# Optimization experiments

Measured on AMD Instinct MI355X. Metric: run time of the kernel, lower is better.

The kernel has to match this reference:

```python
import jax, jax.numpy as jnp
import numpy as np

SPLIT_LEVELS = 3
START_DIM = 0
GROUPS = 8
NUM_RECTS = 2 ** SPLIT_LEVELS


def setup_inputs() -> dict:
    key = jax.random.key(0)
    ks = jax.random.split(key, 10)
    B, N, C, Cin, H, W = 8, 2048, 512, 128, 96, 96
    sd = 0.02
    return {
        'x': jax.random.normal(ks[0], (B, N, C), jnp.float32),
        'r': jax.random.uniform(ks[1], (B, N, 4), jnp.float32),
        'I': jax.random.normal(ks[2], (B, Cin, H, W), jnp.float32),
        'IX': jax.random.normal(ks[3], (B, Cin, H, W), jnp.float32),
        'IY': jax.random.normal(ks[4], (B, Cin, H, W), jnp.float32),
        'IT': jax.random.normal(ks[5], (B, Cin, H, W), jnp.float32),
        'W_ratios': jax.random.normal(ks[6], (C, 2 ** SPLIT_LEVELS - 1), jnp.float32) * sd,
        'b_ratios': jnp.zeros((2 ** SPLIT_LEVELS - 1,), jnp.float32),
        'W_mask': jax.random.normal(ks[7], (C, NUM_RECTS * GROUPS), jnp.float32) * sd,
        'b_mask': jnp.zeros((NUM_RECTS * GROUPS,), jnp.float32),
        'W_samp': jax.random.normal(ks[8], (Cin, C), jnp.float32) * sd,
        'b_samp': jnp.zeros((C,), jnp.float32),
        'ln_g': jnp.ones((C,), jnp.float32),
        'ln_b': jnp.zeros((C,), jnp.float32),
    }


def _topleft(I, IX, IY, IT, x, y):
    # x, y: [B, P] continuous coords; returns [B, Cin, P]
    B, P = x.shape
    Cin = I.shape[1]
    x = x[:, None, :]
    y = y[:, None, :]
    X = jnp.ceil(x).astype(jnp.int32)
    Y = jnp.ceil(y).astype(jnp.int32)
    # torch uses X-1 (wraps at -1) but the matching weight is 0 there, so clamp is equivalent
    Xm = jnp.maximum(X - 1, 0)
    Ym = jnp.maximum(Y - 1, 0)
    z = jnp.zeros_like(X)
    dx = X.astype(x.dtype) - x
    dy = Y.astype(y.dtype) - y
    wx1 = 0.5 * dx ** 2
    wx2 = dx - wx1
    wy1 = 0.5 * dy ** 2
    wy2 = dy - wy1
    b = jnp.arange(B)[:, None, None]
    c = jnp.arange(Cin)[None, :, None]
    g = lambda A, xi, yi: A[b, c, xi, yi]  # gather -> [B, Cin, P]
    s_a = g(IT, X, Y)
    s_e1 = (wy1 * (g(IX, X, Ym) - 0.5 * g(I, X, Ym) - 0.5 * g(I, z, Ym))
            + wy2 * (g(IX, X, Y) - 0.5 * g(I, X, Y) - 0.5 * g(I, z, Y)))
    s_e2 = (wx1 * (g(IY, Xm, Y) - 0.5 * g(I, Xm, Y) - 0.5 * g(I, Xm, z))
            + wx2 * (g(IY, X, Y) - 0.5 * g(I, X, Y) - 0.5 * g(I, X, z)))
    s_c = (wx1 * wy1 * g(I, Xm, Ym) + wx2 * wy1 * g(I, X, Ym)
           + wx1 * wy2 * g(I, Xm, Y) + wx2 * wy2 * g(I, X, Y))
    return s_a - s_e1 - s_e2 + s_c


def _sample_rects(r, I, IX, IY, IT):
    # r: [B, M, rects, 4] normalized rects
    B, M, rects, _ = r.shape
    Cin, H, W = I.shape[1], I.shape[2], I.shape[3]
    fac = jnp.array([H - 1, W - 1, H - 1, W - 1], dtype=r.dtype)
    p = (r * fac).reshape(B, M * rects, 4)
    x1, y1, x2, y2 = p[..., 0], p[..., 1], p[..., 2], p[..., 3]
    tl = lambda xx, yy: _topleft(I, IX, IY, IT, xx, yy)
    S = tl(x2, y2) - tl(x1, y2) - tl(x2, y1) + tl(x1, y1)
    area = jnp.abs((x1 - x2) * (y1 - y2)) + 1e-9
    S = S / area[:, None, :]
    return S.reshape(B, Cin, M, rects).transpose(0, 2, 3, 1)  # [B, M, rects, Cin]


def _forward(x, r, I, IX, IY, IT, W_ratios, b_ratios, W_mask, b_mask, W_samp, b_samp, ln_g, ln_b):
    B, N, C = x.shape
    ratios = jax.nn.sigmoid(x @ W_ratios + b_ratios)  # [B, N, 2^L - 1]
    rr = r[:, :, None, :]  # [B, N, 1, 4]
    level_rects = []
    for i in range(SPLIT_LEVELS):
        dim = (START_DIM + i) % 2
        rat = ratios[:, :, 2 ** i - 1: 2 ** (i + 1) - 1][..., None]  # [B,N,2^i,1]
        p0, p1, p2, p3 = jnp.split(rr, 4, axis=3)
        pos = (p0, p1, p2, p3)
        mid = pos[dim] * (1 - rat) + pos[dim + 2] * rat
        if dim == 0:
            r1 = jnp.concatenate([p0, p1, mid, p3], 3)
            r2 = jnp.concatenate([mid, p1, p2, p3], 3)
        else:
            r1 = jnp.concatenate([p0, p1, p2, mid], 3)
            r2 = jnp.concatenate([p0, mid, p2, p3], 3)
        rr = jnp.concatenate([r1, r2], 2)
        level_rects.append(rr)
    mask = jax.nn.softmax((x @ W_mask + b_mask).reshape(B, N, NUM_RECTS, GROUPS), axis=2)
    S = _sample_rects(rr, I, IX, IY, IT)          # [B, N, rects, Cin]
    s = S @ W_samp + b_samp                        # [B, N, rects, C]
    gc = C // GROUPS
    s = s.reshape(B, N, NUM_RECTS, GROUPS, gc)
    y = jnp.einsum('bnsg,bnsgc->bngc', mask, s).reshape(B, N, C)
    mu = jnp.mean(y, axis=-1, keepdims=True)
    var = jnp.var(y, axis=-1, keepdims=True)
    y = (y - mu) / jnp.sqrt(var + 1e-5) * ln_g + ln_b + x
    return y, level_rects


def reference(x, r, I, IX, IY, IT, W_ratios, b_ratios, W_mask, b_mask, W_samp, b_samp, ln_g, ln_b):
    y, level_rects = _forward(x, r, I, IX, IY, IT, W_ratios, b_ratios, W_mask, b_mask,
                              W_samp, b_samp, ln_g, ln_b)
    return (y, *level_rects)
```

## Files before the change

kernel.cpp:

```cpp
#include <hip/hip_runtime.h>
#include <math.h>

#define B_    8
#define N_    2048
#define C_    512
#define CIN_  128
#define H_    96
#define W_    96
#define HW_   (H_*W_)
#define IMG_  (CIN_*HW_)

#define OUT_L0 (B_*N_*C_)
#define OUT_L1 (OUT_L0 + B_*N_*8)
#define OUT_L2 (OUT_L1 + B_*N_*16)

__device__ __forceinline__ float fm(float a, float b) { return __fmul_rn(a, b); }
__device__ __forceinline__ float fa(float a, float b) { return __fadd_rn(a, b); }
__device__ __forceinline__ float fs(float a, float b) { return __fsub_rn(a, b); }

#define TCH 64
__global__ __launch_bounds__(256) void transpose_kernel(
    const float* __restrict__ I, const float* __restrict__ IX,
    const float* __restrict__ IY, const float* __restrict__ IT,
    float* __restrict__ out)
{
    __shared__ float tile[TCH][97];
    const int x   = blockIdx.x;
    const int b   = blockIdx.y;
    const int z   = blockIdx.z;
    const int img = z >> 1;
    const int ch0 = (z & 1) * TCH;
    const float* src = (img == 0) ? I : (img == 1) ? IX : (img == 2) ? IY : IT;
    const float* sp = src + (size_t)b * IMG_ + (size_t)ch0 * HW_ + (size_t)x * W_;

    for (int i = threadIdx.x; i < TCH * 24; i += 256) {
        const int c = i / 24, qy = i - c * 24;
        const float4 v = *(const float4*)(sp + (size_t)c * HW_ + qy * 4);
        tile[c][qy * 4 + 0] = v.x; tile[c][qy * 4 + 1] = v.y;
        tile[c][qy * 4 + 2] = v.z; tile[c][qy * 4 + 3] = v.w;
    }
    __syncthreads();
    float* op = out + (size_t)img * (B_ * (size_t)HW_ * CIN_)
                    + (size_t)b * ((size_t)HW_ * CIN_)
                    + (size_t)x * (W_ * CIN_) + ch0;
    for (int i = threadIdx.x; i < 96 * 16; i += 256) {
        const int y = i >> 4, cq = i & 15;
        float4 w;
        w.x = tile[cq * 4 + 0][y]; w.y = tile[cq * 4 + 1][y];
        w.z = tile[cq * 4 + 2][y]; w.w = tile[cq * 4 + 3][y];
        *(float4*)(op + (size_t)y * CIN_ + cq * 4) = w;
    }
}

__global__ __launch_bounds__(256) void frontend_kernel(
    const float* __restrict__ x, const float* __restrict__ r,
    const float* __restrict__ Wr, const float* __restrict__ br,
    const float* __restrict__ Wm, const float* __restrict__ bm,
    float* __restrict__ out, float* __restrict__ rects_ws, float* __restrict__ mask_ws)
{
    const int wv   = threadIdx.x >> 6;
    const int lane = threadIdx.x & 63;
    const int row0 = blockIdx.x << 4;
    const int rb   = wv << 2;

    __shared__ __align__(16) float xs[16][C_];
    __shared__ float mlog[16][64];
    __shared__ float ratv[16][7];

    {
        const float4* xp = (const float4*)(x + (size_t)row0 * C_);
        float4* xd = (float4*)xs;
        #pragma unroll
        for (int i = 0; i < 8; ++i) xd[threadIdx.x + i * 256] = xp[threadIdx.x + i * 256];
    }
    __syncthreads();

    {
        const int o = lane;
        float p[4][4];
        #pragma unroll
        for (int rr = 0; rr < 4; ++rr)
            #pragma unroll
            for (int q = 0; q < 4; ++q) p[rr][q] = 0.f;
        #pragma unroll
        for (int q = 0; q < 4; ++q) {
            const float* wp = Wm + (size_t)(q * 128) * 64 + o;
            #pragma unroll 8
            for (int i = 0; i < 128; ++i) {
                const float wm = wp[(size_t)i * 64];
                p[0][q] = fmaf(xs[rb + 0][q * 128 + i], wm, p[0][q]);
                p[1][q] = fmaf(xs[rb + 1][q * 128 + i], wm, p[1][q]);
                p[2][q] = fmaf(xs[rb + 2][q * 128 + i], wm, p[2][q]);
                p[3][q] = fmaf(xs[rb + 3][q * 128 + i], wm, p[3][q]);
            }
        }
        #pragma unroll
        for (int rr = 0; rr < 4; ++rr)
            mlog[rb + rr][o] = fa(fa(fa(fa(p[rr][0], p[rr][1]), p[rr][2]), p[rr][3]), bm[o]);
    }
    if (lane < 32) {
        const int rr = lane >> 3, o = lane & 7;
        if (o < 7) {
            const float* wp = Wr + o;
            const float* xr = xs[rb + rr];
            float p1 = 0.f, p2 = 0.f;
            for (int k = 0; k < 384; ++k)   p1 = fmaf(xr[k], wp[(size_t)k * 7], p1);
            for (int k = 384; k < 512; ++k) p2 = fmaf(xr[k], wp[(size_t)k * 7], p2);
            const float z = fa(fa(p1, p2), br[o]);
            ratv[rb + rr][o] = (float)(1.0 / (1.0 + exp(-(double)z)));
        }
    }
    __syncthreads();

    if (threadIdx.x < 128) {
        const int rr = threadIdx.x >> 3, g = threadIdx.x & 7;
        float mx = -1e30f;
        #pragma unroll
        for (int s = 0; s < 8; ++s) mx = fmaxf(mx, mlog[rr][s * 8 + g]);
        float e[8], sum = 0.f;
        #pragma unroll
        for (int s = 0; s < 8; ++s) { e[s] = expf(mlog[rr][s * 8 + g] - mx); sum += e[s]; }
        const float inv = 1.0f / sum;
        float* mw = mask_ws + (size_t)(row0 + rr) * 64;
        #pragma unroll
        for (int s = 0; s < 8; ++s) mw[s * 8 + g] = e[s] * inv;
    } else if (threadIdx.x < 144) {
        const int rr  = threadIdx.x - 128;
        const int row = row0 + rr;
        float rx1[8], ry1[8], rx2[8], ry2[8];
        const float* rp = r + (size_t)row * 4;
        rx1[0] = rp[0]; ry1[0] = rp[1]; rx2[0] = rp[2]; ry2[0] = rp[3];
        float* lr0 = out + OUT_L0 + (size_t)row * 8;
        float* lr1 = out + OUT_L1 + (size_t)row * 16;
        float* lr2 = out + OUT_L2 + (size_t)row * 32;
        {
            const float t = ratv[rr][0];
            const float m = fa(fm(rx1[0], fs(1.0f, t)), fm(rx2[0], t));
            rx1[1] = m; ry1[1] = ry1[0]; rx2[1] = rx2[0]; ry2[1] = ry2[0];
            rx2[0] = m;
        }
        for (int s = 0; s < 2; ++s) {
            lr0[s*4+0] = rx1[s]; lr0[s*4+1] = ry1[s];
            lr0[s*4+2] = rx2[s]; lr0[s*4+3] = ry2[s];
        }
        for (int j = 0; j < 2; ++j) {
            const float t = ratv[rr][1 + j];
            const float m = fa(fm(ry1[j], fs(1.0f, t)), fm(ry2[j], t));
            rx1[2+j] = rx1[j]; ry1[2+j] = m; rx2[2+j] = rx2[j]; ry2[2+j] = ry2[j];
            ry2[j] = m;
        }
        for (int s = 0; s < 4; ++s) {
            lr1[s*4+0] = rx1[s]; lr1[s*4+1] = ry1[s];
            lr1[s*4+2] = rx2[s]; lr1[s*4+3] = ry2[s];
        }
        for (int j = 0; j < 4; ++j) {
            const float t = ratv[rr][3 + j];
            const float m = fa(fm(rx1[j], fs(1.0f, t)), fm(rx2[j], t));
            rx1[4+j] = m; ry1[4+j] = ry1[j]; rx2[4+j] = rx2[j]; ry2[4+j] = ry2[j];
            rx2[j] = m;
        }
        float* rw = rects_ws + (size_t)row * 32;
        for (int s = 0; s < 8; ++s) {
            lr2[s*4+0] = rx1[s]; lr2[s*4+1] = ry1[s];
            lr2[s*4+2] = rx2[s]; lr2[s*4+3] = ry2[s];
            rw[s*4+0] = rx1[s]; rw[s*4+1] = ry1[s];
            rw[s*4+2] = rx2[s]; rw[s*4+3] = ry2[s];
        }
    }
}

template <bool NHWC>
__device__ __forceinline__ float4 ld4f(const float* __restrict__ p, int xi, int yi, int c0)
{
    if (NHWC) {
        return *(const float4*)(p + ((size_t)(xi * W_ + yi) * CIN_ + c0));
    } else {
        const float* q = p + (size_t)c0 * HW_ + xi * W_ + yi;
        float4 v;
        v.x = q[0]; v.y = q[HW_]; v.z = q[2 * HW_]; v.w = q[3 * HW_];
        return v;
    }
}

__device__ __forceinline__ void sample_one(
    const float* __restrict__ rect, int c0,
    const float* __restrict__ pI, const float* __restrict__ pIX,
    const float* __restrict__ pIY, const float* __restrict__ pIT,
    float* __restrict__ Sout)
{
    const float X1 = fm(rect[0], 95.0f), Y1 = fm(rect[1], 95.0f);
    const float X2 = fm(rect[2], 95.0f), Y2 = fm(rect[3], 95.0f);
    const float area = fa(fabsf(fm(fs(X1, X2), fs(Y1, Y2))), 1e-9f);

    const float uxv[2] = { X2, X1 };
    const float uyv[2] = { Y2, Y1 };
    int UX[2], UXm[2], UY[2], UYm[2];
    float wx1u[2], wx2u[2], wy1u[2], wy2u[2];
    #pragma unroll
    for (int j = 0; j < 2; ++j) {
        const float xcf = ceilf(uxv[j]);
        UX[j] = (int)xcf; UXm[j] = max(UX[j] - 1, 0);
        const float dx = fs(xcf, uxv[j]);
        wx1u[j] = fm(0.5f, fm(dx, dx)); wx2u[j] = fs(dx, wx1u[j]);
        const float ycf = ceilf(uyv[j]);
        UY[j] = (int)ycf; UYm[j] = max(UY[j] - 1, 0);
        const float dy = fs(ycf, uyv[j]);
        wy1u[j] = fm(0.5f, fm(dy, dy)); wy2u[j] = fs(dy, wy1u[j]);
    }

    float4 i_xm0u[2], i_x0u[2], i_0ymu[2], i_0yu[2];
    #pragma unroll
    for (int j = 0; j < 2; ++j) {
        i_xm0u[j] = ld4f<true>(pI, UXm[j], 0, c0);
        i_x0u[j]  = ld4f<true>(pI, UX[j],  0, c0);
        i_0ymu[j] = ld4f<true>(pI, 0, UYm[j], c0);
        i_0yu[j]  = ld4f<true>(pI, 0, UY[j],  c0);
    }
    float4 it_xy[4], ix_xym[4], ix_xy[4], iy_xmy[4], iy_xy[4],
           i_xym[4], i_xy[4], i_xmy[4], i_xmym[4];
    #pragma unroll
    for (int k = 0; k < 4; ++k) {
        const int X = UX[k & 1], Xm = UXm[k & 1];
        const int Y = UY[k >> 1], Ym = UYm[k >> 1];
        it_xy[k]  = ld4f<true>(pIT, X,  Y,  c0);
        ix_xym[k] = ld4f<true>(pIX, X,  Ym, c0);
        ix_xy[k]  = ld4f<true>(pIX, X,  Y,  c0);
        iy_xmy[k] = ld4f<true>(pIY, Xm, Y,  c0);
        iy_xy[k]  = ld4f<true>(pIY, X,  Y,  c0);
        i_xym[k]  = ld4f<true>(pI,  X,  Ym, c0);
        i_xy[k]   = ld4f<true>(pI,  X,  Y,  c0);
        i_xmy[k]  = ld4f<true>(pI,  Xm, Y,  c0);
        i_xmym[k] = ld4f<true>(pI,  Xm, Ym, c0);
    }

    float4 tlv[4];
    #define TLF_BODY(k, f) { \
        const float wx1 = wx1u[(k) & 1], wx2 = wx2u[(k) & 1]; \
        const float wy1 = wy1u[(k) >> 1], wy2 = wy2u[(k) >> 1]; \
        const float t1 = fs(fs(ix_xym[k].f, fm(0.5f, i_xym[k].f)), fm(0.5f, i_0ymu[(k) >> 1].f)); \
        const float t2 = fs(fs(ix_xy[k].f,  fm(0.5f, i_xy[k].f)),  fm(0.5f, i_0yu[(k) >> 1].f)); \
        const float e1 = fa(fm(wy1, t1), fm(wy2, t2)); \
        const float u1 = fs(fs(iy_xmy[k].f, fm(0.5f, i_xmy[k].f)), fm(0.5f, i_xm0u[(k) & 1].f)); \
        const float u2 = fs(fs(iy_xy[k].f,  fm(0.5f, i_xy[k].f)),  fm(0.5f, i_x0u[(k) & 1].f)); \
        const float e2 = fa(fm(wx1, u1), fm(wx2, u2)); \
        const float cc = fa(fa(fa(fm(fm(wx1, wy1), i_xmym[k].f), \
                                   fm(fm(wx2, wy1), i_xym[k].f)), \
                                   fm(fm(wx1, wy2), i_xmy[k].f)), \
                                   fm(fm(wx2, wy2), i_xy[k].f)); \
        tlv[k].f = fa(fs(fs(it_xy[k].f, e1), e2), cc); }
    TLF_BODY(0, x) TLF_BODY(0, y) TLF_BODY(0, z) TLF_BODY(0, w)
    TLF_BODY(1, x) TLF_BODY(1, y) TLF_BODY(1, z) TLF_BODY(1, w)
    TLF_BODY(2, x) TLF_BODY(2, y) TLF_BODY(2, z) TLF_BODY(2, w)
    TLF_BODY(3, x) TLF_BODY(3, y) TLF_BODY(3, z) TLF_BODY(3, w)
    #undef TLF_BODY

    #define SCOMB(f, idx) { \
        const float sc = fa(fs(fs(tlv[0].f, tlv[1].f), tlv[2].f), tlv[3].f); \
        Sout[c0 + idx] = sc / area; }
    SCOMB(x, 0) SCOMB(y, 1) SCOMB(z, 2) SCOMB(w, 3)
    #undef SCOMB
}

__global__ __launch_bounds__(256) void gather5_kernel(
    const float* __restrict__ gI, const float* __restrict__ gIX,
    const float* __restrict__ gIY, const float* __restrict__ gIT,
    const float* __restrict__ rects_ws, const float* __restrict__ mask_ws,
    float* __restrict__ sm_ws)
{
    const int bid   = blockIdx.x;
    const int batch = bid & 7;
    const int row0  = (batch << 11) | ((bid >> 3) << 2);
    const int tid   = threadIdx.x;
    const int rr    = tid >> 6;
    const int c0    = (tid & 63) << 1;

    __shared__ float rect_l[4][32];
    __shared__ float mask_l[4][64];
    if (tid < 128) ((float*)rect_l)[tid] = rects_ws[(size_t)row0 * 32 + tid];
    ((float*)mask_l)[tid] = mask_ws[(size_t)row0 * 64 + tid];
    __syncthreads();

    const float* rl = rect_l[rr];
    const float xt[7] = { rl[0], rl[2], rl[18], rl[6], rl[22], rl[10], rl[14] };
    const float yt[4] = { rl[1], rl[3], rl[7], rl[11] };

    float Xf[7]; int Xc[7], Xm[7]; float wx1v[7], wx2v[7];
    #pragma unroll
    for (int i = 0; i < 7; ++i) {
        Xf[i] = fm(xt[i], 95.0f);
        const float cf = ceilf(Xf[i]);
        Xc[i] = (int)cf; Xm[i] = max(Xc[i] - 1, 0);
        const float dx = fs(cf, Xf[i]);
        wx1v[i] = fm(0.5f, fm(dx, dx)); wx2v[i] = fs(dx, wx1v[i]);
    }
    float Yf[4]; int Yc[4], Ymv[4]; float wy1v[4], wy2v[4];
    #pragma unroll
    for (int i = 0; i < 4; ++i) {
        Yf[i] = fm(yt[i], 95.0f);
        const float cf = ceilf(Yf[i]);
        Yc[i] = (int)cf; Ymv[i] = max(Yc[i] - 1, 0);
        const float dy = fs(cf, Yf[i]);
        wy1v[i] = fm(0.5f, fm(dy, dy)); wy2v[i] = fs(dy, wy1v[i]);
    }

    const size_t bb = (size_t)batch * IMG_;
    const float* pI  = gI  + bb;
    const float* pIX = gIX + bb;
    const float* pIY = gIY + bb;
    const float* pIT = gIT + bb;

    float2 tl[18];
    #define LD2(p, xi, yi) (*(const float2*)((p) + ((size_t)((xi) * W_ + (yi)) * CIN_ + c0)))
    #define TLC(P, f) { \
        const float t1 = fs(fs(ix_xym.f, fm(0.5f, i_xym.f)), fm(0.5f, i_0ym.f)); \
        const float t2 = fs(fs(ix_xy.f,  fm(0.5f, i_xy.f)),  fm(0.5f, i_0y.f)); \
        const float e1 = fa(fm(wy1, t1), fm(wy2, t2)); \
        const float u1 = fs(fs(iy_xmy.f, fm(0.5f, i_xmy.f)), fm(0.5f, i_xm0.f)); \
        const float u2 = fs(fs(iy_xy.f,  fm(0.5f, i_xy.f)),  fm(0.5f, i_x0.f)); \
        const float e2 = fa(fm(wx1, u1), fm(wx2, u2)); \
        const float cc = fa(fa(fa(fm(fm(wx1, wy1), i_xmym.f), \
                                   fm(fm(wx2, wy1), i_xym.f)), \
                                   fm(fm(wx1, wy2), i_xmy.f)), \
                                   fm(fm(wx2, wy2), i_xy.f)); \
        tl[P].f = fa(fs(fs(it_xy.f, e1), e2), cc); }
    #define PT(P, XI, YI) { \
        const int X = Xc[XI], Xmm = Xm[XI], Y = Yc[YI], Ymm = Ymv[YI]; \
        const float wx1 = wx1v[XI], wx2 = wx2v[XI], wy1 = wy1v[YI], wy2 = wy2v[YI]; \
        const float2 it_xy  = LD2(pIT, X,   Y); \
        const float2 ix_xym = LD2(pIX, X,   Ymm); \
        const float2 ix_xy  = LD2(pIX, X,   Y); \
        const float2 iy_xmy = LD2(pIY, Xmm, Y); \
        const float2 iy_xy  = LD2(pIY, X,   Y); \
        const float2 i_xym  = LD2(pI,  X,   Ymm); \
        const float2 i_0ym  = LD2(pI,  0,   Ymm); \
        const float2 i_xy   = LD2(pI,  X,   Y); \
        const float2 i_0y   = LD2(pI,  0,   Y); \
        const float2 i_xmy  = LD2(pI,  Xmm, Y); \
        const float2 i_xm0  = LD2(pI,  Xmm, 0); \
        const float2 i_x0   = LD2(pI,  X,   0); \
        const float2 i_xmym = LD2(pI,  Xmm, Ymm); \
        TLC(P, x) TLC(P, y) }

    PT(0, 0, 0) PT(1, 1, 0) PT(2, 2, 0) PT(5, 0, 1) PT(6, 1, 1) PT(7, 2, 1)
    PT(3, 3, 0) PT(4, 4, 0) PT(9, 2, 2) PT(10, 3, 2) PT(11, 4, 2)
    PT(8, 5, 1) PT(13, 0, 3) PT(14, 2, 3) PT(15, 5, 3)
    PT(12, 6, 2) PT(16, 6, 3) PT(17, 4, 3)
    #undef PT
    #undef TLC
    #undef LD2

    float2 S[8];
    #define AREA(x1i, y1i, x2i, y2i) \
        fa(fabsf(fm(fs(Xf[x1i], Xf[x2i]), fs(Yf[y1i], Yf[y2i]))), 1e-9f)
    #define COMB(s, A, Bp, Cp, D, x1i, y1i, x2i, y2i) { \
        const float ar = AREA(x1i, y1i, x2i, y2i); \
        S[s].x = fa(fs(fs(tl[A].x, tl[Bp].x), tl[Cp].x), tl[D].x) / ar; \
        S[s].y = fa(fs(fs(tl[A].y, tl[Bp].y), tl[Cp].y), tl[D].y) / ar; }
    COMB(0,  6,  5,  1,  0,  0, 0, 1, 1)
    COMB(1, 10,  9,  3,  2,  2, 0, 3, 2)
    COMB(2, 15, 13,  8,  5,  0, 1, 5, 3)
    COMB(3, 16, 14, 12,  9,  2, 2, 6, 3)
    COMB(4,  7,  6,  2,  1,  1, 0, 2, 1)
    COMB(5, 11, 10,  4,  3,  3, 0, 4, 2)
    COMB(6, 14, 15,  7,  8,  5, 1, 2, 3)
    COMB(7, 17, 16, 11, 12,  6, 2, 4, 3)
    #undef COMB
    #undef AREA

    const float* mk = mask_l[rr];
    float* smp = sm_ws + (size_t)(row0 + rr) * 1024 + c0;
    #pragma unroll
    for (int g = 0; g < 8; ++g) {
        float ax = 0.f, ay = 0.f;
        #pragma unroll
        for (int s = 0; s < 8; ++s) {
            const float m = mk[s * 8 + g];
            ax = fmaf(m, S[s].x, ax);
            ay = fmaf(m, S[s].y, ay);
        }
        *(float2*)(smp + g * 128) = make_float2(ax, ay);
    }
}

#define R78 16
__global__ __launch_bounds__(256) void stage78_kernel(
    const float* __restrict__ x,
    const float* __restrict__ Ws, const float* __restrict__ bs,
    const float* __restrict__ lng, const float* __restrict__ lnb,
    const float* __restrict__ sm_ws, float* __restrict__ out)
{
    const int row0 = blockIdx.x * R78;
    const int tid  = threadIdx.x;

    __shared__ __align__(16) float SM_l[R78][8][CIN_];
    __shared__ float red[R78][4][2];
    __shared__ float stats[R78][2];

    {
        const float4* src = (const float4*)(sm_ws + (size_t)row0 * 1024);
        float4* dst = (float4*)SM_l;
        #pragma unroll
        for (int k = 0; k < 16; ++k) dst[tid + k * 256] = src[tid + k * 256];
    }
    __syncthreads();

    const int o0 = tid, o1 = tid + 256;
    const int g0 = o0 >> 6, g1 = o1 >> 6;
    float a0[R78], a1[R78];
    {
        const float b0 = bs[o0], b1 = bs[o1];
        #pragma unroll
        for (int q = 0; q < R78; ++q) { a0[q] = b0; a1[q] = b1; }
    }
    const float* w0 = Ws + o0;
    #pragma unroll 4
    for (int c = 0; c < 128; ++c) {
        const float wa = w0[(size_t)c * 512];
        const float wb = w0[(size_t)c * 512 + 256];
        #pragma unroll
        for (int q = 0; q < R78; ++q) {
            a0[q] = fmaf(SM_l[q][g0][c], wa, a0[q]);
            a1[q] = fmaf(SM_l[q][g1][c], wb, a1[q]);
        }
    }
    const int wv = tid >> 6, lane = tid & 63;
    #pragma unroll
    for (int q = 0; q < R78; ++q) {
        float s1 = a0[q] + a1[q];
        float s2 = fmaf(a0[q], a0[q], a1[q] * a1[q]);
        #pragma unroll
        for (int off = 32; off > 0; off >>= 1) {
            s1 += __shfl_down(s1, off);
            s2 += __shfl_down(s2, off);
        }
        if (lane == 0) { red[q][wv][0] = s1; red[q][wv][1] = s2; }
    }
    __syncthreads();
    if (tid < R78) {
        float t1 = 0.f, t2 = 0.f;
        #pragma unroll
        for (int w = 0; w < 4; ++w) { t1 += red[tid][w][0]; t2 += red[tid][w][1]; }
        const float mu  = t1 * (1.0f / 512.0f);
        const float var = t2 * (1.0f / 512.0f) - mu * mu;
        stats[tid][0] = mu; stats[tid][1] = rsqrtf(var + 1e-5f);
    }
    __syncthreads();
    const float lg0 = lng[o0], lb0 = lnb[o0];
    const float lg1 = lng[o1], lb1 = lnb[o1];
    #pragma unroll
    for (int q = 0; q < R78; ++q) {
        const size_t rowb = (size_t)(row0 + q) * C_;
        const float mu = stats[q][0], rstd = stats[q][1];
        out[rowb + o0] = (a0[q] - mu) * rstd * lg0 + lb0 + x[rowb + o0];
        out[rowb + o1] = (a1[q] - mu) * rstd * lg1 + lb1 + x[rowb + o1];
    }
}

__global__ __launch_bounds__(512) void gather_kernel(
    const float* __restrict__ x,
    const float* __restrict__ Ws, const float* __restrict__ bs,
    const float* __restrict__ lng, const float* __restrict__ lnb,
    const float* __restrict__ gI, const float* __restrict__ gIX,
    const float* __restrict__ gIY, const float* __restrict__ gIT,
    const float* __restrict__ rects_ws, const float* __restrict__ mask_ws,
    float* __restrict__ out)
{
    const int bid   = blockIdx.x;
    const int batch = bid & 7;
    const int row0  = (batch << 11) | ((bid >> 3) << 2);
    const int tid   = threadIdx.x;

    __shared__ __align__(16) float xs[4][C_];
    __shared__ float mask_s[4][64];
    __shared__ float rects[4][8][4];
    __shared__ __align__(16) float S_s[4][8][CIN_];
    __shared__ __align__(16) float SM_s[4][8][CIN_];
    __shared__ __align__(16) float yv[4][C_];
    __shared__ float red2[4][8][2];
    __shared__ float stats[4][2];

    {
        const int rr = tid >> 7, q = tid & 127;
        ((float4*)xs[rr])[q] = ((const float4*)(x + (size_t)(row0 + rr) * C_))[q];
    }
    if (tid < 128)      ((float*)rects)[tid] = rects_ws[(size_t)row0 * 32 + tid];
    else if (tid < 384) ((float*)mask_s)[tid - 128] = mask_ws[(size_t)row0 * 64 + (tid - 128)];
    __syncthreads();

    {
        const size_t bb = (size_t)batch * IMG_;
        const float* pI  = gI  + bb;
        const float* pIX = gIX + bb;
        const float* pIY = gIY + bb;
        const float* pIT = gIT + bb;
        #pragma unroll
        for (int it = 0; it < 2; ++it) {
            const int t  = tid + (it << 9);
            const int rr = t >> 8;
            const int s  = (t >> 5) & 7;
            const int c0 = (t & 31) << 2;
            sample_one(rects[rr][s], c0, pI, pIX, pIY, pIT, S_s[rr][s]);
        }
    }
    __syncthreads();

    {
        const int rr = tid >> 7, c = tid & 127;
        #pragma unroll
        for (int g = 0; g < 8; ++g) {
            float acc = 0.f;
            #pragma unroll
            for (int s = 0; s < 8; ++s)
                acc = fmaf(mask_s[rr][s * 8 + g], S_s[rr][s][c], acc);
            SM_s[rr][g][c] = acc;
        }
    }
    __syncthreads();

    {
        const int o = tid;
        const int g = o >> 6;
        float a0 = bs[o], a1 = a0, a2 = a0, a3 = a0;
        const float* w0 = Ws + o;
        #pragma unroll 4
        for (int c = 0; c < 128; ++c) {
            const float w = w0[(size_t)c * 512];
            a0 = fmaf(SM_s[0][g][c], w, a0);
            a1 = fmaf(SM_s[1][g][c], w, a1);
            a2 = fmaf(SM_s[2][g][c], w, a2);
            a3 = fmaf(SM_s[3][g][c], w, a3);
        }
        yv[0][o] = a0; yv[1][o] = a1; yv[2][o] = a2; yv[3][o] = a3;
    }
    __syncthreads();

    {
        const int o = tid, wvv = tid >> 6, lane = tid & 63;
        float v[4], s1[4], s2[4];
        #pragma unroll
        for (int rr = 0; rr < 4; ++rr) {
            v[rr]  = yv[rr][o];
            s1[rr] = v[rr];
            s2[rr] = v[rr] * v[rr];
        }
        #pragma unroll
        for (int off = 32; off > 0; off >>= 1) {
            #pragma unroll
            for (int rr = 0; rr < 4; ++rr) {
                s1[rr] += __shfl_down(s1[rr], off);
                s2[rr] += __shfl_down(s2[rr], off);
            }
        }
        if (lane == 0) {
            #pragma unroll
            for (int rr = 0; rr < 4; ++rr) {
                red2[rr][wvv][0] = s1[rr];
                red2[rr][wvv][1] = s2[rr];
            }
        }
        __syncthreads();
        if (tid < 4) {
            float t1 = 0.f, t2 = 0.f;
            #pragma unroll
            for (int w = 0; w < 8; ++w) { t1 += red2[tid][w][0]; t2 += red2[tid][w][1]; }
            const float mu  = t1 * (1.0f / 512.0f);
            const float var = t2 * (1.0f / 512.0f) - mu * mu;
            stats[tid][0] = mu; stats[tid][1] = rsqrtf(var + 1e-5f);
        }
        __syncthreads();
        const float lg = lng[o], lb = lnb[o];
        #pragma unroll
        for (int rr = 0; rr < 4; ++rr) {
            out[(size_t)(row0 + rr) * C_ + o] =
                (v[rr] - stats[rr][0]) * stats[rr][1] * lg + lb + xs[rr][o];
        }
    }
}

template <bool NHWC>
__global__ __launch_bounds__(256) void fused_kernel(
    const float* __restrict__ x, const float* __restrict__ r,
    const float* __restrict__ Wr, const float* __restrict__ br,
    const float* __restrict__ Wm, const float* __restrict__ bm,
    const float* __restrict__ Ws, const float* __restrict__ bs,
    const float* __restrict__ lng, const float* __restrict__ lnb,
    const float* __restrict__ gI, const float* __restrict__ gIX,
    const float* __restrict__ gIY, const float* __restrict__ gIT,
    float* __restrict__ out)
{
    const int row = blockIdx.x;
    const int b   = row >> 11;
    const int tid = threadIdx.x;

    __shared__ __align__(16) float xs[C_];
    __shared__ float mpart[4][64];
    __shared__ float mlog[64];
    __shared__ float ratv[7];
    __shared__ float mask_s[64];
    __shared__ float rects[8][4];
    __shared__ __align__(16) float S_s[8][CIN_];
    __shared__ __align__(16) float SM_s[8][CIN_];
    __shared__ __align__(16) float yv[C_];
    __shared__ float red[8];
    __shared__ float stats[2];

    if (tid < 128) ((float4*)xs)[tid] = ((const float4*)(x + (size_t)row * C_))[tid];
    __syncthreads();

    {
        const int o = tid & 63, q = tid >> 6;
        const float* wp = Wm + (size_t)(q * 128) * 64 + o;
        float acc = 0.f;
        #pragma unroll 8
        for (int i = 0; i < 128; ++i) acc = fmaf(xs[q * 128 + i], wp[(size_t)i * 64], acc);
        mpart[q][o] = acc;
    }
    if (tid >= 64 && tid < 71) {
        const int o = tid - 64;
        const float* wp = Wr + o;
        float p1 = 0.f, p2 = 0.f;
        for (int k = 0; k < 384; ++k)   p1 = fmaf(xs[k], wp[(size_t)k * 7], p1);
        for (int k = 384; k < 512; ++k) p2 = fmaf(xs[k], wp[(size_t)k * 7], p2);
        const float z = fa(fa(p1, p2), br[o]);
        ratv[o] = (float)(1.0 / (1.0 + exp(-(double)z)));
    }
    __syncthreads();

    if (tid < 64)
        mlog[tid] = fa(fa(fa(fa(mpart[0][tid], mpart[1][tid]), mpart[2][tid]), mpart[3][tid]), bm[tid]);
    __syncthreads();

    if (tid < 8) {
        const int g = tid;
        float mx = -1e30f;
        #pragma unroll
        for (int s = 0; s < 8; ++s) mx = fmaxf(mx, mlog[s * 8 + g]);
        float e[8], sum = 0.f;
        #pragma unroll
        for (int s = 0; s < 8; ++s) { e[s] = expf(mlog[s * 8 + g] - mx); sum += e[s]; }
        const float inv = 1.0f / sum;
        #pragma unroll
        for (int s = 0; s < 8; ++s) mask_s[s * 8 + g] = e[s] * inv;
    }
    if (tid == 64) {
        float rx1[8], ry1[8], rx2[8], ry2[8];
        const float* rp = r + (size_t)row * 4;
        rx1[0] = rp[0]; ry1[0] = rp[1]; rx2[0] = rp[2]; ry2[0] = rp[3];
        float* lr0 = out + OUT_L0 + (size_t)row * 8;
        float* lr1 = out + OUT_L1 + (size_t)row * 16;
        float* lr2 = out + OUT_L2 + (size_t)row * 32;
        {
            const float t = ratv[0];
            const float m = fa(fm(rx1[0], fs(1.0f, t)), fm(rx2[0], t));
            rx1[1] = m; ry1[1] = ry1[0]; rx2[1] = rx2[0]; ry2[1] = ry2[0];
            rx2[0] = m;
        }
        for (int s = 0; s < 2; ++s) {
            lr0[s*4+0] = rx1[s]; lr0[s*4+1] = ry1[s];
            lr0[s*4+2] = rx2[s]; lr0[s*4+3] = ry2[s];
        }
        for (int j = 0; j < 2; ++j) {
            const float t = ratv[1 + j];
            const float m = fa(fm(ry1[j], fs(1.0f, t)), fm(ry2[j], t));
            rx1[2+j] = rx1[j]; ry1[2+j] = m; rx2[2+j] = rx2[j]; ry2[2+j] = ry2[j];
            ry2[j] = m;
        }
        for (int s = 0; s < 4; ++s) {
            lr1[s*4+0] = rx1[s]; lr1[s*4+1] = ry1[s];
            lr1[s*4+2] = rx2[s]; lr1[s*4+3] = ry2[s];
        }
        for (int j = 0; j < 4; ++j) {
            const float t = ratv[3 + j];
            const float m = fa(fm(rx1[j], fs(1.0f, t)), fm(rx2[j], t));
            rx1[4+j] = m; ry1[4+j] = ry1[j]; rx2[4+j] = rx2[j]; ry2[4+j] = ry2[j];
            rx2[j] = m;
        }
        for (int s = 0; s < 8; ++s) {
            lr2[s*4+0] = rx1[s]; lr2[s*4+1] = ry1[s];
            lr2[s*4+2] = rx2[s]; lr2[s*4+3] = ry2[s];
            rects[s][0] = rx1[s]; rects[s][1] = ry1[s];
            rects[s][2] = rx2[s]; rects[s][3] = ry2[s];
        }
    }
    __syncthreads();

    {
        const int s  = tid >> 5;
        const int c0 = (tid & 31) << 2;
        const size_t bb = (size_t)b * IMG_;
        if (NHWC) {
            sample_one(rects[s], c0, gI + bb, gIX + bb, gIY + bb, gIT + bb, S_s[s]);
        } else {
            const float X1 = fm(rects[s][0], 95.0f), Y1 = fm(rects[s][1], 95.0f);
            const float X2 = fm(rects[s][2], 95.0f), Y2 = fm(rects[s][3], 95.0f);
            const float area = fa(fabsf(fm(fs(X1, X2), fs(Y1, Y2))), 1e-9f);
            const float* pI  = gI  + bb;
            const float* pIX = gIX + bb;
            const float* pIY = gIY + bb;
            const float* pIT = gIT + bb;
            const float cx[4] = { X2, X1, X2, X1 };
            const float cy[4] = { Y2, Y2, Y1, Y1 };
            float4 tlv[4];
            #pragma unroll
            for (int k = 0; k < 4; ++k) {
                const float xx = cx[k], yy = cy[k];
                const float xcf = ceilf(xx), ycf = ceilf(yy);
                const int X = (int)xcf, Y = (int)ycf;
                const int Xm = max(X - 1, 0), Ym = max(Y - 1, 0);
                const float dx = fs(xcf, xx), dy = fs(ycf, yy);
                const float wx1 = fm(0.5f, fm(dx, dx)), wx2 = fs(dx, wx1);
                const float wy1 = fm(0.5f, fm(dy, dy)), wy2 = fs(dy, wy1);

                const float4 it_xy  = ld4f<NHWC>(pIT, X,  Y,  c0);
                const float4 ix_xym = ld4f<NHWC>(pIX, X,  Ym, c0);
                const float4 ix_xy  = ld4f<NHWC>(pIX, X,  Y,  c0);
                const float4 iy_xmy = ld4f<NHWC>(pIY, Xm, Y,  c0);
                const float4 iy_xy  = ld4f<NHWC>(pIY, X,  Y,  c0);
                const float4 i_xym  = ld4f<NHWC>(pI,  X,  Ym, c0);
                const float4 i_0ym  = ld4f<NHWC>(pI,  0,  Ym, c0);
                const float4 i_xy   = ld4f<NHWC>(pI,  X,  Y,  c0);
                const float4 i_0y   = ld4f<NHWC>(pI,  0,  Y,  c0);
                const float4 i_xmy  = ld4f<NHWC>(pI,  Xm, Y,  c0);
                const float4 i_xm0  = ld4f<NHWC>(pI,  Xm, 0,  c0);
                const float4 i_x0   = ld4f<NHWC>(pI,  X,  0,  c0);
                const float4 i_xmym = ld4f<NHWC>(pI,  Xm, Ym, c0);

                #define TLF(f) { \
                    const float t1 = fs(fs(ix_xym.f, fm(0.5f, i_xym.f)), fm(0.5f, i_0ym.f)); \
                    const float t2 = fs(fs(ix_xy.f,  fm(0.5f, i_xy.f)),  fm(0.5f, i_0y.f)); \
                    const float e1 = fa(fm(wy1, t1), fm(wy2, t2)); \
                    const float u1 = fs(fs(iy_xmy.f, fm(0.5f, i_xmy.f)), fm(0.5f, i_xm0.f)); \
                    const float u2 = fs(fs(iy_xy.f,  fm(0.5f, i_xy.f)),  fm(0.5f, i_x0.f)); \
                    const float e2 = fa(fm(wx1, u1), fm(wx2, u2)); \
                    const float cc = fa(fa(fa(fm(fm(wx1, wy1), i_xmym.f), \
                                               fm(fm(wx2, wy1), i_xym.f)), \
                                               fm(fm(wx1, wy2), i_xmy.f)), \
                                               fm(fm(wx2, wy2), i_xy.f)); \
                    tlv[k].f = fa(fs(fs(it_xy.f, e1), e2), cc); }
                TLF(x) TLF(y) TLF(z) TLF(w)
                #undef TLF
            }
            #define SCOMB(f, idx) { \
                const float sc = fa(fs(fs(tlv[0].f, tlv[1].f), tlv[2].f), tlv[3].f); \
                S_s[s][c0 + idx] = sc / area; }
            SCOMB(x, 0) SCOMB(y, 1) SCOMB(z, 2) SCOMB(w, 3)
            #undef SCOMB
        }
    }
    __syncthreads();

    {
        const int c = tid & 127;
        #pragma unroll
        for (int p = 0; p < 4; ++p) {
            const int g = (tid >> 7) + p * 2;
            float acc = 0.f;
            #pragma unroll
            for (int s = 0; s < 8; ++s) acc = fmaf(mask_s[s * 8 + g], S_s[s][c], acc);
            SM_s[g][c] = acc;
        }
    }
    __syncthreads();

    {
        float a0 = bs[tid], a1 = bs[tid + 256];
        const int g0 = tid >> 6;
        const int g1 = g0 + 4;
        const float* w0 = Ws + tid;
        #pragma unroll 4
        for (int c = 0; c < 128; ++c) {
            a0 = fmaf(SM_s[g0][c], w0[(size_t)c * 512],       a0);
            a1 = fmaf(SM_s[g1][c], w0[(size_t)c * 512 + 256], a1);
        }
        yv[tid] = a0; yv[tid + 256] = a1;
    }
    __syncthreads();

    {
        const float v0 = yv[tid], v1 = yv[tid + 256];
        float s1 = v0 + v1, s2 = fmaf(v0, v0, v1 * v1);
        #pragma unroll
        for (int off = 32; off > 0; off >>= 1) {
            s1 += __shfl_down(s1, off);
            s2 += __shfl_down(s2, off);
        }
        if ((tid & 63) == 0) { red[(tid >> 6) * 2] = s1; red[(tid >> 6) * 2 + 1] = s2; }
        __syncthreads();
        if (tid == 0) {
            const float t1 = red[0] + red[2] + red[4] + red[6];
            const float t2 = red[1] + red[3] + red[5] + red[7];
            const float mu = t1 * (1.0f / 512.0f);
            const float var = t2 * (1.0f / 512.0f) - mu * mu;
            stats[0] = mu; stats[1] = rsqrtf(var + 1e-5f);
        }
        __syncthreads();
        const float mu = stats[0], rstd = stats[1];
        float* op = out + (size_t)row * C_;
        op[tid]       = (v0 - mu) * rstd * lng[tid]       + lnb[tid]       + xs[tid];
        op[tid + 256] = (v1 - mu) * rstd * lng[tid + 256] + lnb[tid + 256] + xs[tid + 256];
    }
}

extern "C" void kernel_launch(void* const* d_in, const int* in_sizes, int n_in,
                              void* d_out, int out_size, void* d_ws, size_t ws_size,
                              hipStream_t stream)
{
    const float* x   = (const float*)d_in[0];
    const float* r   = (const float*)d_in[1];
    const float* I   = (const float*)d_in[2];
    const float* IX  = (const float*)d_in[3];
    const float* IY  = (const float*)d_in[4];
    const float* IT  = (const float*)d_in[5];
    const float* Wr  = (const float*)d_in[6];
    const float* br  = (const float*)d_in[7];
    const float* Wm  = (const float*)d_in[8];
    const float* bm  = (const float*)d_in[9];
    const float* Ws  = (const float*)d_in[10];
    const float* bs  = (const float*)d_in[11];
    const float* lng = (const float*)d_in[12];
    const float* lnb = (const float*)d_in[13];
    float* out = (float*)d_out;

    const size_t img_elems  = (size_t)B_ * HW_ * CIN_;
    const size_t need_img   = 4 * img_elems * sizeof(float);
    const size_t fe_elems   = (size_t)B_ * N_ * (32 + 64);
    const size_t sm_elems   = (size_t)B_ * N_ * 1024;
    const size_t need_split = need_img + fe_elems * sizeof(float);
    const size_t need_full  = need_split + sm_elems * sizeof(float);

    if (ws_size >= need_full) {
        float* T        = (float*)d_ws;
        float* rects_ws = T + 4 * img_elems;
        float* mask_ws  = rects_ws + (size_t)B_ * N_ * 32;
        float* sm_ws    = mask_ws + (size_t)B_ * N_ * 64;
        dim3 tg(H_, B_, 8);
        transpose_kernel<<<tg, 256, 0, stream>>>(I, IX, IY, IT, T);
        frontend_kernel<<<B_ * N_ / 16, 256, 0, stream>>>(
            x, r, Wr, br, Wm, bm, out, rects_ws, mask_ws);
        gather5_kernel<<<B_ * N_ / 4, 256, 0, stream>>>(
            T, T + img_elems, T + 2 * img_elems, T + 3 * img_elems,
            rects_ws, mask_ws, sm_ws);
        stage78_kernel<<<B_ * N_ / R78, 256, 0, stream>>>(
            x, Ws, bs, lng, lnb, sm_ws, out);
    } else if (ws_size >= need_split) {
        float* T        = (float*)d_ws;
        float* rects_ws = T + 4 * img_elems;
        float* mask_ws  = rects_ws + (size_t)B_ * N_ * 32;
        dim3 tg(H_, B_, 8);
        transpose_kernel<<<tg, 256, 0, stream>>>(I, IX, IY, IT, T);
        frontend_kernel<<<B_ * N_ / 16, 256, 0, stream>>>(
            x, r, Wr, br, Wm, bm, out, rects_ws, mask_ws);
        gather_kernel<<<B_ * N_ / 4, 512, 0, stream>>>(
            x, Ws, bs, lng, lnb,
            T, T + img_elems, T + 2 * img_elems, T + 3 * img_elems,
            rects_ws, mask_ws, out);
    } else if (ws_size >= need_img) {
        float* T = (float*)d_ws;
        dim3 tg(H_, B_, 8);
        transpose_kernel<<<tg, 256, 0, stream>>>(I, IX, IY, IT, T);
        fused_kernel<true><<<B_ * N_, 256, 0, stream>>>(
            x, r, Wr, br, Wm, bm, Ws, bs, lng, lnb,
            T, T + img_elems, T + 2 * img_elems, T + 3 * img_elems, out);
    } else {
        fused_kernel<false><<<B_ * N_, 256, 0, stream>>>(
            x, r, Wr, br, Wm, bm, Ws, bs, lng, lnb,
            I, IX, IY, IT, out);
    }
}
```

Baseline: 506.3 us.

## Fuse transpose and frontend into one kernel; register-tile stage78 GEMM with float4

The image transpose and the frontend (mask logits, ratios, rect splitting) now run as one interleaved launch. Every seventh block does frontend work and the rest do transpose tiles, so the two independent workloads overlap and one launch is saved. The stage78 projection plus LayerNorm is restructured so each thread computes 4 contiguous output channels for 8 rows, using float4 weight loads and padded shared memory. This raises arithmetic intensity and vectorizes the output stores, but increases register pressure and shared-memory footprint for the fused kernel.

```diff
diff --git a/kernel.cpp b/kernel.cpp
--- a/kernel.cpp
+++ b/kernel.cpp
@@ -19,6 +19,162 @@
 __device__ __forceinline__ float fs(float a, float b) { return __fsub_rn(a, b); }
 
 #define TCH 64
+
+__global__ __launch_bounds__(256) void prep_kernel(
+    const float* __restrict__ I, const float* __restrict__ IX,
+    const float* __restrict__ IY, const float* __restrict__ IT,
+    float* __restrict__ T,
+    const float* __restrict__ x, const float* __restrict__ r,
+    const float* __restrict__ Wr, const float* __restrict__ br,
+    const float* __restrict__ Wm, const float* __restrict__ bm,
+    float* __restrict__ out, float* __restrict__ rects_ws, float* __restrict__ mask_ws)
+{
+    __shared__ __align__(16) float smem[16 * C_ + 16 * 64 + 16 * 8];
+    const int bid = blockIdx.x;
+
+    if (bid % 7 != 0) {
+        const int t   = bid - bid / 7 - 1;
+        const int xh  = t % 96;
+        const int b   = (t / 96) & 7;
+        const int z   = t / 768;
+        const int img = z >> 1;
+        const int ch0 = (z & 1) * TCH;
+        float (*tile)[97] = (float(*)[97])smem;
+
+        const float* src = (img == 0) ? I : (img == 1) ? IX : (img == 2) ? IY : IT;
+        const float* sp = src + (size_t)b * IMG_ + (size_t)ch0 * HW_ + (size_t)xh * W_;
+
+        for (int i = threadIdx.x; i < TCH * 24; i += 256) {
+            const int c = i / 24, qy = i - c * 24;
+            const float4 v = *(const float4*)(sp + (size_t)c * HW_ + qy * 4);
+            tile[c][qy * 4 + 0] = v.x; tile[c][qy * 4 + 1] = v.y;
+            tile[c][qy * 4 + 2] = v.z; tile[c][qy * 4 + 3] = v.w;
+        }
+        __syncthreads();
+        float* op = T + (size_t)img * (B_ * (size_t)HW_ * CIN_)
+                      + (size_t)b * ((size_t)HW_ * CIN_)
+                      + (size_t)xh * (W_ * CIN_) + ch0;
+        for (int i = threadIdx.x; i < 96 * 16; i += 256) {
+            const int y = i >> 4, cq = i & 15;
+            float4 w;
+            w.x = tile[cq * 4 + 0][y]; w.y = tile[cq * 4 + 1][y];
+            w.z = tile[cq * 4 + 2][y]; w.w = tile[cq * 4 + 3][y];
+            *(float4*)(op + (size_t)y * CIN_ + cq * 4) = w;
+        }
+        return;
+    }
+
+    float (*xs)[C_]  = (float(*)[C_])smem;
+    float (*mlog)[64] = (float(*)[64])(smem + 16 * C_);
+    float (*ratv)[8]  = (float(*)[8])(smem + 16 * C_ + 16 * 64);
+
+    const int wv   = threadIdx.x >> 6;
+    const int lane = threadIdx.x & 63;
+    const int row0 = (bid / 7) << 4;
+    const int rb   = wv << 2;
+
+    {
+        const float4* xp = (const float4*)(x + (size_t)row0 * C_);
+        float4* xd = (float4*)xs;
+        #pragma unroll
+        for (int i = 0; i < 8; ++i) xd[threadIdx.x + i * 256] = xp[threadIdx.x + i * 256];
+    }
+    __syncthreads();
+
+    {
+        const int o = lane;
+        float p[4][4];
+        #pragma unroll
+        for (int rr = 0; rr < 4; ++rr)
+            #pragma unroll
+            for (int q = 0; q < 4; ++q) p[rr][q] = 0.f;
+        #pragma unroll
+        for (int q = 0; q < 4; ++q) {
+            const float* wp = Wm + (size_t)(q * 128) * 64 + o;
+            #pragma unroll 8
+            for (int i = 0; i < 128; ++i) {
+                const float wm = wp[(size_t)i * 64];
+                p[0][q] = fmaf(xs[rb + 0][q * 128 + i], wm, p[0][q]);
+                p[1][q] = fmaf(xs[rb + 1][q * 128 + i], wm, p[1][q]);
+                p[2][q] = fmaf(xs[rb + 2][q * 128 + i], wm, p[2][q]);
+                p[3][q] = fmaf(xs[rb + 3][q * 128 + i], wm, p[3][q]);
+            }
+        }
+        #pragma unroll
+        for (int rr = 0; rr < 4; ++rr)
+            mlog[rb + rr][o] = fa(fa(fa(fa(p[rr][0], p[rr][1]), p[rr][2]), p[rr][3]), bm[o]);
+    }
+    if (lane < 32) {
+        const int rr = lane >> 3, o = lane & 7;
+        if (o < 7) {
+            const float* wp = Wr + o;
+            const float* xr = xs[rb + rr];
+            float p1 = 0.f, p2 = 0.f;
+            for (int k = 0; k < 384; ++k)   p1 = fmaf(xr[k], wp[(size_t)k * 7], p1);
+            for (int k = 384; k < 512; ++k) p2 = fmaf(xr[k], wp[(size_t)k * 7], p2);
+            const float z = fa(fa(p1, p2), br[o]);
+            ratv[rb + rr][o] = (float)(1.0 / (1.0 + exp(-(double)z)));
+        }
+    }
+    __syncthreads();
+
+    if (threadIdx.x < 128) {
+        const int rr = threadIdx.x >> 3, g = threadIdx.x & 7;
+        float mx = -1e30f;
+        #pragma unroll
+        for (int s = 0; s < 8; ++s) mx = fmaxf(mx, mlog[rr][s * 8 + g]);
+        float e[8], sum = 0.f;
+        #pragma unroll
+        for (int s = 0; s < 8; ++s) { e[s] = expf(mlog[rr][s * 8 + g] - mx); sum += e[s]; }
+        const float inv = 1.0f / sum;
+        float* mw = mask_ws + (size_t)(row0 + rr) * 64;
+        #pragma unroll
+        for (int s = 0; s < 8; ++s) mw[s * 8 + g] = e[s] * inv;
+    } else if (threadIdx.x < 144) {
+        const int rr  = threadIdx.x - 128;
+        const int row = row0 + rr;
+        float rx1[8], ry1[8], rx2[8], ry2[8];
+        const float* rp = r + (size_t)row * 4;
+        rx1[0] = rp[0]; ry1[0] = rp[1]; rx2[0] = rp[2]; ry2[0] = rp[3];
+        float* lr0 = out + OUT_L0 + (size_t)row * 8;
+        float* lr1 = out + OUT_L1 + (size_t)row * 16;
+        float* lr2 = out + OUT_L2 + (size_t)row * 32;
+        {
+            const float t = ratv[rr][0];
+            const float m = fa(fm(rx1[0], fs(1.0f, t)), fm(rx2[0], t));
+            rx1[1] = m; ry1[1] = ry1[0]; rx2[1] = rx2[0]; ry2[1] = ry2[0];
+            rx2[0] = m;
+        }
+        for (int s = 0; s < 2; ++s) {
+            lr0[s*4+0] = rx1[s]; lr0[s*4+1] = ry1[s];
+            lr0[s*4+2] = rx2[s]; lr0[s*4+3] = ry2[s];
+        }
+        for (int j = 0; j < 2; ++j) {
+            const float t = ratv[rr][1 + j];
+            const float m = fa(fm(ry1[j], fs(1.0f, t)), fm(ry2[j], t));
+            rx1[2+j] = rx1[j]; ry1[2+j] = m; rx2[2+j] = rx2[j]; ry2[2+j] = ry2[j];
+            ry2[j] = m;
+        }
+        for (int s = 0; s < 4; ++s) {
+            lr1[s*4+0] = rx1[s]; lr1[s*4+1] = ry1[s];
+            lr1[s*4+2] = rx2[s]; lr1[s*4+3] = ry2[s];
+        }
+        for (int j = 0; j < 4; ++j) {
+            const float t = ratv[rr][3 + j];
+            const float m = fa(fm(rx1[j], fs(1.0f, t)), fm(rx2[j], t));
+            rx1[4+j] = m; ry1[4+j] = ry1[j]; rx2[4+j] = rx2[j]; ry2[4+j] = ry2[j];
+            rx2[j] = m;
+        }
+        float* rw = rects_ws + (size_t)row * 32;
+        for (int s = 0; s < 8; ++s) {
+            lr2[s*4+0] = rx1[s]; lr2[s*4+1] = ry1[s];
+            lr2[s*4+2] = rx2[s]; lr2[s*4+3] = ry2[s];
+            rw[s*4+0] = rx1[s]; rw[s*4+1] = ry1[s];
+            rw[s*4+2] = rx2[s]; rw[s*4+3] = ry2[s];
+        }
+    }
+}
+
 __global__ __launch_bounds__(256) void transpose_kernel(
     const float* __restrict__ I, const float* __restrict__ IX,
     const float* __restrict__ IY, const float* __restrict__ IT,
@@ -391,68 +547,99 @@
 {
     const int row0 = blockIdx.x * R78;
     const int tid  = threadIdx.x;
-
-    __shared__ __align__(16) float SM_l[R78][8][CIN_];
-    __shared__ float red[R78][4][2];
+    const int half = tid >> 7;
+    const int grp  = tid & 127;
+    const int o    = grp << 2;
+    const int g    = grp >> 4;
+
+    __shared__ __align__(16) float SM_l[R78][8][132];
+    __shared__ float red[R78][2][2];
     __shared__ float stats[R78][2];
 
     {
         const float4* src = (const float4*)(sm_ws + (size_t)row0 * 1024);
-        float4* dst = (float4*)SM_l;
-        #pragma unroll
-        for (int k = 0; k < 16; ++k) dst[tid + k * 256] = src[tid + k * 256];
-    }
-    __syncthreads();
-
-    const int o0 = tid, o1 = tid + 256;
-    const int g0 = o0 >> 6, g1 = o1 >> 6;
-    float a0[R78], a1[R78];
-    {
-        const float b0 = bs[o0], b1 = bs[o1];
-        #pragma unroll
-        for (int q = 0; q < R78; ++q) { a0[q] = b0; a1[q] = b1; }
-    }
-    const float* w0 = Ws + o0;
-    #pragma unroll 4
-    for (int c = 0; c < 128; ++c) {
-        const float wa = w0[(size_t)c * 512];
-        const float wb = w0[(size_t)c * 512 + 256];
-        #pragma unroll
-        for (int q = 0; q < R78; ++q) {
-            a0[q] = fmaf(SM_l[q][g0][c], wa, a0[q]);
-            a1[q] = fmaf(SM_l[q][g1][c], wb, a1[q]);
-        }
-    }
-    const int wv = tid >> 6, lane = tid & 63;
+        #pragma unroll
+        for (int k = 0; k < 16; ++k) {
+            const int idx = tid + (k << 8);
+            const int q   = idx >> 8;
+            const int gg  = (idx >> 5) & 7;
+            const int c4  = idx & 31;
+            ((float4*)&SM_l[q][gg][0])[c4] = src[idx];
+        }
+    }
+    __syncthreads();
+
+    const int qb = half << 3;
+    float4 a[8];
+    {
+        const float4 b4 = *(const float4*)(bs + o);
+        #pragma unroll
+        for (int q = 0; q < 8; ++q) a[q] = b4;
+    }
+    #pragma unroll 2
+    for (int c4 = 0; c4 < 32; ++c4) {
+        float4 w0 = *(const float4*)(Ws + (size_t)(c4 * 4 + 0) * 512 + o);
+        float4 w1 = *(const float4*)(Ws + (size_t)(c4 * 4 + 1) * 512 + o);
+        float4 w2 = *(const float4*)(Ws + (size_t)(c4 * 4 + 2) * 512 + o);
+        float4 w3 = *(const float4*)(Ws + (size_t)(c4 * 4 + 3) * 512 + o);
+        #pragma unroll
+        for (int q = 0; q < 8; ++q) {
+            const float4 sv = ((const float4*)&SM_l[qb + q][g][0])[c4];
+            a[q].x = fmaf(sv.x, w0.x, a[q].x);
+            a[q].x = fmaf(sv.y, w1.x, a[q].x);
+            a[q].x = fmaf(sv.z, w2.x, a[q].x);
+            a[q].x = fmaf(sv.w, w3.x, a[q].x);
+            a[q].y = fmaf(sv.x, w0.y, a[q].y);
+            a[q].y = fmaf(sv.y, w1.y, a[q].y);
+            a[q].y = fmaf(sv.z, w2.y, a[q].y);
+            a[q].y = fmaf(sv.w, w3.y, a[q].y);
+            a[q].z = fmaf(sv.x, w0.z, a[q].z);
+            a[q].z = fmaf(sv.y, w1.z, a[q].z);
+            a[q].z = fmaf(sv.z, w2.z, a[q].z);
+            a[q].z = fmaf(sv.w, w3.z, a[q].z);
+            a[q].w = fmaf(sv.x, w0.w, a[q].w);
+            a[q].w = fmaf(sv.y, w1.w, a[q].w);
+            a[q].w = fmaf(sv.z, w2.w, a[q].w);
+            a[q].w = fmaf(sv.w, w3.w, a[q].w);
+        }
+    }
+
+    const int wv   = tid >> 6;
+    const int lane = tid & 63;
     #pragma unroll
-    for (int q = 0; q < R78; ++q) {
-        float s1 = a0[q] + a1[q];
-        float s2 = fmaf(a0[q], a0[q], a1[q] * a1[q]);
+    for (int q = 0; q < 8; ++q) {
+        float s1 = ((a[q].x + a[q].y) + a[q].z) + a[q].w;
+        float s2 = fmaf(a[q].x, a[q].x, fmaf(a[q].y, a[q].y,
+                   fmaf(a[q].z, a[q].z, a[q].w * a[q].w)));
         #pragma unroll
         for (int off = 32; off > 0; off >>= 1) {
             s1 += __shfl_down(s1, off);
             s2 += __shfl_down(s2, off);
         }
-        if (lane == 0) { red[q][wv][0] = s1; red[q][wv][1] = s2; }
+        if (lane == 0) { red[qb + q][wv & 1][0] = s1; red[qb + q][wv & 1][1] = s2; }
     }
     __syncthreads();
     if (tid < R78) {
-        float t1 = 0.f, t2 = 0.f;
-        #pragma unroll
-        for (int w = 0; w < 4; ++w) { t1 += red[tid][w][0]; t2 += red[tid][w][1]; }
+        const float t1 = red[tid][0][0] + red[tid][1][0];
+        const float t2 = red[tid][0][1] + red[tid][1][1];
         const float mu  = t1 * (1.0f / 512.0f);
         const float var = t2 * (1.0f / 512.0f) - mu * mu;
         stats[tid][0] = mu; stats[tid][1] = rsqrtf(var + 1e-5f);
     }
     __syncthreads();
-    const float lg0 = lng[o0], lb0 = lnb[o0];
-    const float lg1 = lng[o1], lb1 = lnb[o1];
+    const float4 lg = *(const float4*)(lng + o);
+    const float4 lb = *(const float4*)(lnb + o);
     #pragma unroll
-    for (int q = 0; q < R78; ++q) {
-        const size_t rowb = (size_t)(row0 + q) * C_;
-        const float mu = stats[q][0], rstd = stats[q][1];
-        out[rowb + o0] = (a0[q] - mu) * rstd * lg0 + lb0 + x[rowb + o0];
-        out[rowb + o1] = (a1[q] - mu) * rstd * lg1 + lb1 + x[rowb + o1];
+    for (int q = 0; q < 8; ++q) {
+        const int row = row0 + qb + q;
+        const float mu = stats[qb + q][0], rstd = stats[qb + q][1];
+        const float4 xv = *(const float4*)(x + (size_t)row * C_ + o);
+        float4 ov;
+        ov.x = (a[q].x - mu) * rstd * lg.x + lb.x + xv.x;
+        ov.y = (a[q].y - mu) * rstd * lg.y + lb.y + xv.y;
+        ov.z = (a[q].z - mu) * rstd * lg.z + lb.z + xv.z;
+        ov.w = (a[q].w - mu) * rstd * lg.w + lb.w + xv.w;
+        *(float4*)(out + (size_t)row * C_ + o) = ov;
     }
 }
 
@@ -833,9 +1020,8 @@
         float* rects_ws = T + 4 * img_elems;
         float* mask_ws  = rects_ws + (size_t)B_ * N_ * 32;
         float* sm_ws    = mask_ws + (size_t)B_ * N_ * 64;
-        dim3 tg(H_, B_, 8);
-        transpose_kernel<<<tg, 256, 0, stream>>>(I, IX, IY, IT, T);
-        frontend_kernel<<<B_ * N_ / 16, 256, 0, stream>>>(
+        prep_kernel<<<7168, 256, 0, stream>>>(
+            I, IX, IY, IT, T,
             x, r, Wr, br, Wm, bm, out, rects_ws, mask_ws);
         gather5_kernel<<<B_ * N_ / 4, 256, 0, stream>>>(
             T, T + img_elems, T + 2 * img_elems, T + 3 * img_elems,
```

Result: faster. 479.3 us (-5.3%).
